# Kernel optimization log

Measured on AMD Instinct MI355X. Metric: run time of the kernel, lower is better.

Reference implementation:

```python
import jax, jax.numpy as jnp
import numpy as np

KS, STRIDE, DIL = 5, 1, 1
PAD = (KS + (KS - 1) * (DIL - 1) - 1) // 2
EPS = 1e-5


def _unfold_t(x):
    # x: (N, C, T, V) -> (N, C, T_out, KS, V), zero-padded temporal windows
    N, C, T, V = x.shape
    xp = jnp.pad(x, ((0, 0), (0, 0), (PAD, PAD), (0, 0)))
    t_out = (T + 2 * PAD - DIL * (KS - 1) - 1) // STRIDE + 1
    idx = jnp.arange(t_out)[:, None] * STRIDE + jnp.arange(KS)[None, :] * DIL  # (T_out, KS)
    return xp[:, :, idx, :]


def _bn2d(x, g, b):
    # training-mode BatchNorm2d: biased batch stats over (N, T, V)
    mu = jnp.mean(x, axis=(0, 2, 3), keepdims=True)
    var = jnp.var(x, axis=(0, 2, 3), keepdims=True)
    xn = (x - mu) * jax.lax.rsqrt(var + EPS)
    return xn * g[None, :, None, None] + b[None, :, None, None]


def setup_inputs() -> dict:
    key = jax.random.key(0)
    ks = jax.random.split(key, 8)
    N, C, T, V = 64, 64, 128, 25
    R, O = 8, 128
    s = 0.05
    return {
        "x": jax.random.normal(ks[0], (N, C, T, V), jnp.float32),
        "Wv": jax.random.normal(ks[1], (R, C), jnp.float32) * s,
        "bv": jax.random.normal(ks[2], (R,), jnp.float32) * s,
        "Ww": jax.random.normal(ks[3], (KS * KS, KS), jnp.float32) * s,
        "bw": jax.random.normal(ks[4], (KS * KS,), jnp.float32) * s,
        "g_bn": jnp.ones((R,), jnp.float32),
        "b_bn": jnp.zeros((R,), jnp.float32),
        "Wr": jax.random.normal(ks[5], (R, C), jnp.float32) * s,
        "br": jax.random.normal(ks[6], (R,), jnp.float32) * s,
        "g_r": jnp.ones((R,), jnp.float32),
        "b_r": jnp.zeros((R,), jnp.float32),
        "Wo": jax.random.normal(ks[7], (O, R), jnp.float32) * s,
        "bo": jnp.zeros((O,), jnp.float32),
        "g_o": jnp.ones((O,), jnp.float32),
        "b_o": jnp.zeros((O,), jnp.float32),
    }


def reference(x, Wv, bv, Ww, bw, g_bn, b_bn, Wr, br, g_r, b_r, Wo, bo, g_o, b_o):
    N, C, T, V = x.shape
    # convV (1x1) then unfold both x and v
    v0 = jnp.einsum('rc,nctv->nrtv', Wv, x) + bv[None, :, None, None]
    xu = _unfold_t(x)      # (N, C, T, W, V)
    vu = _unfold_t(v0)     # (N, R, T, W, V)
    # mean over channels, move window dim to channel position for convW
    m = jnp.mean(xu, axis=1).transpose(0, 2, 1, 3)  # (N, W, T, V)
    w = jnp.einsum('ow,nwtv->notv', Ww, m) + bw[None, :, None, None]
    weights = jnp.tanh(w.reshape(N, KS, KS, T, V))  # (N, W, W, T, V)
    att = jnp.einsum('nwutv,nctuv->nctv', weights, vu)  # (N, R, T, V)
    # residual 1x1 conv + BN (in_channels != out_channels -> conv path)
    res = _bn2d(jnp.einsum('rc,nctv->nrtv', Wr, x) + br[None, :, None, None], g_r, b_r)
    h = _bn2d(att, g_bn, b_bn) + res
    h = jnp.where(h >= 0, h, 0.1 * h)  # LeakyReLU(0.1)
    out = _bn2d(jnp.einsum('or,nrtv->notv', Wo, h) + bo[None, :, None, None], g_o, b_o)
    return out
```

## Files before the change

### kernel.cpp

```cpp
#include <hip/hip_runtime.h>
#include <math.h>

#define TV 3200
#define NTV 204800
#define NB 800
constexpr float EPSF = 1e-5f;

template<int NS>
__device__ inline void write_partials(float (&vals)[NS], float* __restrict__ out, float* lds){
  int lane = threadIdx.x & 63;
  int wid  = threadIdx.x >> 6;
  #pragma unroll
  for (int s = 0; s < NS; ++s){
    float v = vals[s];
    #pragma unroll
    for (int o = 32; o > 0; o >>= 1) v += __shfl_down(v, o);
    if (lane == 0) lds[s*4 + wid] = v;
  }
  __syncthreads();
  if ((int)threadIdx.x < NS){
    float v = lds[threadIdx.x*4+0] + lds[threadIdx.x*4+1]
            + lds[threadIdx.x*4+2] + lds[threadIdx.x*4+3];
    out[threadIdx.x*NB + blockIdx.x] = v;
  }
}

__global__ __launch_bounds__(256) void k_proj(const float* __restrict__ x,
    const float* __restrict__ Wv, const float* __restrict__ bv,
    const float* __restrict__ Wr, const float* __restrict__ br,
    float* __restrict__ v0, float* __restrict__ r0, float* __restrict__ s,
    float* __restrict__ pr){
  __shared__ float sWv[512], sWr[512], lds[16*4];
  int tid = threadIdx.x;
  for (int i = tid; i < 512; i += 256){ sWv[i] = Wv[i]; sWr[i] = Wr[i]; }
  __syncthreads();
  int p = blockIdx.x*256 + tid;
  int n = p / TV, tv = p - n*TV;
  const float* xp = x + (size_t)n*64*TV + tv;
  float av[8] = {0,0,0,0,0,0,0,0};
  float ar[8] = {0,0,0,0,0,0,0,0};
  float ssum = 0.f;
  for (int c = 0; c < 64; ++c){
    float xv = xp[(size_t)c*TV];
    ssum += xv;
    #pragma unroll
    for (int r = 0; r < 8; ++r){
      av[r] = fmaf(sWv[r*64+c], xv, av[r]);
      ar[r] = fmaf(sWr[r*64+c], xv, ar[r]);
    }
  }
  s[p] = ssum * 0.015625f;
  float* v0p = v0 + (size_t)n*8*TV + tv;
  float* r0p = r0 + (size_t)n*8*TV + tv;
  float vals[16];
  #pragma unroll
  for (int r = 0; r < 8; ++r){
    v0p[(size_t)r*TV] = av[r] + bv[r];
    float rr = ar[r] + br[r];
    r0p[(size_t)r*TV] = rr;
    vals[r] = rr; vals[8+r] = rr*rr;
  }
  write_partials<16>(vals, pr, lds);
}

__global__ __launch_bounds__(256) void k_w2(const float* __restrict__ s,
    const float* __restrict__ Ww, const float* __restrict__ bw,
    float* __restrict__ W2){
  __shared__ float sWw[125], sbw[25];
  int tid = threadIdx.x;
  if (tid < 125) sWw[tid] = Ww[tid];
  if (tid < 25)  sbw[tid] = bw[tid];
  __syncthreads();
  int p = blockIdx.x*256 + tid;
  int n = p / TV, tv = p - n*TV;
  int t = tv / 25, v = tv - t*25;
  float m[5];
  #pragma unroll
  for (int k = 0; k < 5; ++k){
    int tt = t + k - 2;
    m[k] = (tt >= 0 && tt < 128) ? s[n*TV + tt*25 + v] : 0.f;
  }
  float w2[5] = {0,0,0,0,0};
  #pragma unroll
  for (int w = 0; w < 5; ++w){
    #pragma unroll
    for (int u = 0; u < 5; ++u){
      int o = w*5 + u;
      float wo = sbw[o];
      #pragma unroll
      for (int k = 0; k < 5; ++k) wo = fmaf(sWw[o*5+k], m[k], wo);
      w2[u] += tanhf(wo);
    }
  }
  float* W2p = W2 + (size_t)n*5*TV + tv;
  #pragma unroll
  for (int u = 0; u < 5; ++u) W2p[(size_t)u*TV] = w2[u];
}

__global__ __launch_bounds__(256) void k_att(const float* __restrict__ W2,
    const float* __restrict__ v0, float* __restrict__ att, float* __restrict__ patt){
  __shared__ float lds[16*4];
  int tid = threadIdx.x;
  int p = blockIdx.x*256 + tid;
  int n = p / TV, tv = p - n*TV;
  int t = tv / 25, v = tv - t*25;
  float a[8] = {0,0,0,0,0,0,0,0};
  const float* W2p = W2 + (size_t)n*5*TV + tv;
  const float* v0n = v0 + (size_t)n*8*TV;
  #pragma unroll
  for (int u = 0; u < 5; ++u){
    int tt = t + u - 2;
    if (tt >= 0 && tt < 128){
      float wu = W2p[(size_t)u*TV];
      const float* vp = v0n + tt*25 + v;
      #pragma unroll
      for (int r = 0; r < 8; ++r) a[r] = fmaf(wu, vp[(size_t)r*TV], a[r]);
    }
  }
  float* ap = att + (size_t)n*8*TV + tv;
  float vals[16];
  #pragma unroll
  for (int r = 0; r < 8; ++r){
    ap[(size_t)r*TV] = a[r];
    vals[r] = a[r]; vals[8+r] = a[r]*a[r];
  }
  write_partials<16>(vals, patt, lds);
}

__global__ __launch_bounds__(256) void k_bncoef(const float* __restrict__ pr,
    const float* __restrict__ patt,
    const float* __restrict__ g_bn, const float* __restrict__ b_bn,
    const float* __restrict__ g_r, const float* __restrict__ b_r,
    float* __restrict__ coef){
  __shared__ float lds[8];
  int b = blockIdx.x;
  bool isatt = (b >= 8);
  int r = isatt ? b - 8 : b;
  const float* ps = (isatt ? patt : pr) + r*NB;
  const float* pq = (isatt ? patt : pr) + (8+r)*NB;
  float s1 = 0.f, s2 = 0.f;
  for (int i = threadIdx.x; i < NB; i += 256){ s1 += ps[i]; s2 += pq[i]; }
  int lane = threadIdx.x & 63, wid = threadIdx.x >> 6;
  #pragma unroll
  for (int o = 32; o > 0; o >>= 1){ s1 += __shfl_down(s1, o); s2 += __shfl_down(s2, o); }
  if (lane == 0){ lds[wid] = s1; lds[4+wid] = s2; }
  __syncthreads();
  if (threadIdx.x == 0){
    float sum = lds[0]+lds[1]+lds[2]+lds[3];
    float sq  = lds[4]+lds[5]+lds[6]+lds[7];
    float mu  = sum / (float)NTV;
    float var = sq / (float)NTV - mu*mu;
    float g  = isatt ? g_bn[r] : g_r[r];
    float bb = isatt ? b_bn[r] : b_r[r];
    float a = g * rsqrtf(var + EPSF);
    float c = bb - a*mu;
    int base = isatt ? 0 : 16;
    coef[base + r] = a;
    coef[base + 8 + r] = c;
  }
}

__global__ __launch_bounds__(256) void k_h(const float* __restrict__ att,
    const float* __restrict__ r0, const float* __restrict__ coef,
    float* __restrict__ h, float* __restrict__ ph){
  __shared__ float lds[44*4];
  __shared__ float sc[32];
  int tid = threadIdx.x;
  if (tid < 32) sc[tid] = coef[tid];
  __syncthreads();
  int p = blockIdx.x*256 + tid;
  int n = p / TV, tv = p - n*TV;
  const float* ap = att + (size_t)n*8*TV + tv;
  const float* rp = r0  + (size_t)n*8*TV + tv;
  float* hp = h + (size_t)n*8*TV + tv;
  float hv[8];
  #pragma unroll
  for (int r = 0; r < 8; ++r){
    float z = sc[r]*ap[(size_t)r*TV] + sc[8+r] + sc[16+r]*rp[(size_t)r*TV] + sc[24+r];
    hv[r] = (z >= 0.f) ? z : 0.1f*z;
    hp[(size_t)r*TV] = hv[r];
  }
  float vals[44];
  #pragma unroll
  for (int r = 0; r < 8; ++r) vals[r] = hv[r];
  int cnt = 8;
  #pragma unroll
  for (int r = 0; r < 8; ++r){
    #pragma unroll
    for (int r2 = r; r2 < 8; ++r2) vals[cnt++] = hv[r]*hv[r2];
  }
  write_partials<44>(vals, ph, lds);
}

__global__ __launch_bounds__(256) void k_hred(const float* __restrict__ ph,
    float* __restrict__ hstat){
  __shared__ float lds[4];
  int j = blockIdx.x;
  float s1 = 0.f;
  for (int i = threadIdx.x; i < NB; i += 256) s1 += ph[j*NB + i];
  int lane = threadIdx.x & 63, wid = threadIdx.x >> 6;
  #pragma unroll
  for (int o = 32; o > 0; o >>= 1) s1 += __shfl_down(s1, o);
  if (lane == 0) lds[wid] = s1;
  __syncthreads();
  if (threadIdx.x == 0) hstat[j] = lds[0]+lds[1]+lds[2]+lds[3];
}

__global__ __launch_bounds__(128) void k_fold(const float* __restrict__ hstat,
    const float* __restrict__ Wo, const float* __restrict__ bo,
    const float* __restrict__ g_o, const float* __restrict__ b_o,
    float* __restrict__ fold, float* __restrict__ bfold){
  __shared__ double muh[8];
  __shared__ double exx[8][8];
  int o = threadIdx.x;
  if (o < 8) muh[o] = (double)hstat[o] / (double)NTV;
  if (o == 0){
    int cnt = 8;
    for (int r = 0; r < 8; ++r)
      for (int r2 = r; r2 < 8; ++r2){
        double e = (double)hstat[cnt++] / (double)NTV;
        exx[r][r2] = e; exx[r2][r] = e;
      }
  }
  __syncthreads();
  double w[8];
  for (int r = 0; r < 8; ++r) w[r] = (double)Wo[o*8+r];
  double bob = (double)bo[o];
  double mu = bob;
  for (int r = 0; r < 8; ++r) mu += w[r]*muh[r];
  double t = 0.0;
  for (int r = 0; r < 8; ++r)
    for (int r2 = 0; r2 < 8; ++r2) t += w[r]*w[r2]*exx[r][r2];
  double ey2 = t + 2.0*bob*(mu - bob) + bob*bob;
  double var = ey2 - mu*mu;
  double a = (double)g_o[o] / sqrt(var + (double)EPSF);
  for (int r = 0; r < 8; ++r) fold[o*8+r] = (float)(a * w[r]);
  bfold[o] = (float)(a * (bob - mu) + (double)b_o[o]);
}

__global__ __launch_bounds__(256) void k_out(const float* __restrict__ h,
    const float* __restrict__ fold, const float* __restrict__ bfold,
    float* __restrict__ out){
  __shared__ float sW[1024], sB[128];
  int tid = threadIdx.x;
  for (int i = tid; i < 1024; i += 256) sW[i] = fold[i];
  if (tid < 128) sB[tid] = bfold[tid];
  __syncthreads();
  int p = blockIdx.x*256 + tid;
  int n = p / TV, tv = p - n*TV;
  const float* hp = h + (size_t)n*8*TV + tv;
  float hv[8];
  #pragma unroll
  for (int r = 0; r < 8; ++r) hv[r] = hp[(size_t)r*TV];
  float* op = out + (size_t)n*128*TV + tv;
  #pragma unroll 4
  for (int o = 0; o < 128; ++o){
    float y = sB[o];
    #pragma unroll
    for (int r = 0; r < 8; ++r) y = fmaf(sW[o*8+r], hv[r], y);
    op[(size_t)o*TV] = y;
  }
}

extern "C" void kernel_launch(void* const* d_in, const int* in_sizes, int n_in,
                              void* d_out, int out_size, void* d_ws, size_t ws_size,
                              hipStream_t stream){
  const float* x    = (const float*)d_in[0];
  const float* Wv   = (const float*)d_in[1];
  const float* bv   = (const float*)d_in[2];
  const float* Ww   = (const float*)d_in[3];
  const float* bw   = (const float*)d_in[4];
  const float* g_bn = (const float*)d_in[5];
  const float* b_bn = (const float*)d_in[6];
  const float* Wr   = (const float*)d_in[7];
  const float* br   = (const float*)d_in[8];
  const float* g_r  = (const float*)d_in[9];
  const float* b_r  = (const float*)d_in[10];
  const float* Wo   = (const float*)d_in[11];
  const float* bo   = (const float*)d_in[12];
  const float* g_o  = (const float*)d_in[13];
  const float* b_o  = (const float*)d_in[14];

  float* ws = (float*)d_ws;
  size_t off = 0;
  float* v0   = ws + off; off += 1638400;
  float* r0   = ws + off; off += 1638400;
  float* s    = ws + off; off += 204800;
  float* W2   = ws + off; off += 1024000;
  float* att  = ws + off; off += 1638400;
  float* hbuf = ws + off; off += 1638400;
  float* pr   = ws + off; off += 16*NB;
  float* patt = ws + off; off += 16*NB;
  float* ph   = ws + off; off += 44*NB;
  float* coef = ws + off; off += 32;
  float* hstat= ws + off; off += 44;
  float* fold = ws + off; off += 1024;
  float* bfold= ws + off; off += 128;

  k_proj  <<<NB, 256, 0, stream>>>(x, Wv, bv, Wr, br, v0, r0, s, pr);
  k_w2    <<<NB, 256, 0, stream>>>(s, Ww, bw, W2);
  k_att   <<<NB, 256, 0, stream>>>(W2, v0, att, patt);
  k_bncoef<<<16, 256, 0, stream>>>(pr, patt, g_bn, b_bn, g_r, b_r, coef);
  k_h     <<<NB, 256, 0, stream>>>(att, r0, coef, hbuf, ph);
  k_hred  <<<44, 256, 0, stream>>>(ph, hstat);
  k_fold  <<<1, 128, 0, stream>>>(hstat, Wo, bo, g_o, b_o, fold, bfold);
  k_out   <<<NB, 256, 0, stream>>>(hbuf, fold, bfold, (float*)d_out);
}
```

Baseline: 240.7 us.

## Fuse attention-weight and attention kernels, vectorize with float4, merge reductions

Fuses the tanh weight computation into the attention kernel using an LDS tile of s and v0 with halo, removing the W2 intermediate buffer. Vectorizes the projection, h and output kernels to process four positions per thread with float4 loads and stores, and splits the output kernel across a second grid dimension over output channels. Merges the h-statistics reduction into the fold kernel, removing a launch. This cuts global traffic and launch count, at the cost of fewer blocks, more registers per thread and redundant halo loads.

```diff
diff --git a/kernel.cpp b/kernel.cpp
--- a/kernel.cpp
+++ b/kernel.cpp
@@ -3,128 +3,154 @@
 
 #define TV 3200
 #define NTV 204800
-#define NB 800
+#define NB 400
 constexpr float EPSF = 1e-5f;
 
 template<int NS>
-__device__ inline void write_partials(float (&vals)[NS], float* __restrict__ out, float* lds){
-  int lane = threadIdx.x & 63;
-  int wid  = threadIdx.x >> 6;
-  #pragma unroll
-  for (int s = 0; s < NS; ++s){
-    float v = vals[s];
+__device__ inline void partials2(const float (&vals)[NS], float* lds, float* out, int ncols){
+  int lane = threadIdx.x & 63, wid = threadIdx.x >> 6;
+  #pragma unroll
+  for (int j = 0; j < NS; ++j){
+    float v = vals[j];
     #pragma unroll
     for (int o = 32; o > 0; o >>= 1) v += __shfl_down(v, o);
-    if (lane == 0) lds[s*4 + wid] = v;
-  }
-  __syncthreads();
-  if ((int)threadIdx.x < NS){
-    float v = lds[threadIdx.x*4+0] + lds[threadIdx.x*4+1]
-            + lds[threadIdx.x*4+2] + lds[threadIdx.x*4+3];
-    out[threadIdx.x*NB + blockIdx.x] = v;
-  }
-}
-
-__global__ __launch_bounds__(256) void k_proj(const float* __restrict__ x,
-    const float* __restrict__ Wv, const float* __restrict__ bv,
+    if (lane == 0) lds[j*2 + wid] = v;
+  }
+  __syncthreads();
+  if ((int)threadIdx.x < NS)
+    out[threadIdx.x*ncols + blockIdx.x] = lds[threadIdx.x*2] + lds[threadIdx.x*2 + 1];
+}
+
+__global__ __launch_bounds__(128, 2) void k_proj(
+    const float* __restrict__ x, const float* __restrict__ Wv, const float* __restrict__ bv,
     const float* __restrict__ Wr, const float* __restrict__ br,
     float* __restrict__ v0, float* __restrict__ r0, float* __restrict__ s,
     float* __restrict__ pr){
-  __shared__ float sWv[512], sWr[512], lds[16*4];
-  int tid = threadIdx.x;
-  for (int i = tid; i < 512; i += 256){ sWv[i] = Wv[i]; sWr[i] = Wr[i]; }
-  __syncthreads();
-  int p = blockIdx.x*256 + tid;
-  int n = p / TV, tv = p - n*TV;
-  const float* xp = x + (size_t)n*64*TV + tv;
-  float av[8] = {0,0,0,0,0,0,0,0};
-  float ar[8] = {0,0,0,0,0,0,0,0};
-  float ssum = 0.f;
+  __shared__ __align__(16) float sW[1024];
+  __shared__ float lds[32];
+  const int tid = threadIdx.x;
+  for (int i = tid; i < 1024; i += 128){
+    int c = i >> 4, j = i & 15;
+    sW[i] = (j < 8) ? Wv[j*64 + c] : Wr[(j-8)*64 + c];
+  }
+  __syncthreads();
+  const int p4 = (blockIdx.x*128 + tid) * 4;
+  const int n = p4 / TV, tv4 = p4 - n*TV;
+  const float* xb = x + (size_t)n*64*TV + tv4;
+  float4 av[8], ar[8];
+  #pragma unroll
+  for (int r = 0; r < 8; ++r){
+    av[r] = make_float4(0.f,0.f,0.f,0.f);
+    ar[r] = make_float4(0.f,0.f,0.f,0.f);
+  }
+  float4 ss = make_float4(0.f,0.f,0.f,0.f);
+  #pragma unroll 8
   for (int c = 0; c < 64; ++c){
-    float xv = xp[(size_t)c*TV];
-    ssum += xv;
+    float4 xv = *(const float4*)(xb + (size_t)c*TV);
+    ss.x += xv.x; ss.y += xv.y; ss.z += xv.z; ss.w += xv.w;
     #pragma unroll
     for (int r = 0; r < 8; ++r){
-      av[r] = fmaf(sWv[r*64+c], xv, av[r]);
-      ar[r] = fmaf(sWr[r*64+c], xv, ar[r]);
-    }
-  }
-  s[p] = ssum * 0.015625f;
-  float* v0p = v0 + (size_t)n*8*TV + tv;
-  float* r0p = r0 + (size_t)n*8*TV + tv;
+      float wv = sW[c*16 + r], wr = sW[c*16 + 8 + r];
+      av[r].x = fmaf(wv, xv.x, av[r].x); av[r].y = fmaf(wv, xv.y, av[r].y);
+      av[r].z = fmaf(wv, xv.z, av[r].z); av[r].w = fmaf(wv, xv.w, av[r].w);
+      ar[r].x = fmaf(wr, xv.x, ar[r].x); ar[r].y = fmaf(wr, xv.y, ar[r].y);
+      ar[r].z = fmaf(wr, xv.z, ar[r].z); ar[r].w = fmaf(wr, xv.w, ar[r].w);
+    }
+  }
+  *(float4*)(s + p4) = make_float4(ss.x*0.015625f, ss.y*0.015625f, ss.z*0.015625f, ss.w*0.015625f);
   float vals[16];
   #pragma unroll
   for (int r = 0; r < 8; ++r){
-    v0p[(size_t)r*TV] = av[r] + bv[r];
-    float rr = ar[r] + br[r];
-    r0p[(size_t)r*TV] = rr;
-    vals[r] = rr; vals[8+r] = rr*rr;
-  }
-  write_partials<16>(vals, pr, lds);
-}
-
-__global__ __launch_bounds__(256) void k_w2(const float* __restrict__ s,
-    const float* __restrict__ Ww, const float* __restrict__ bw,
-    float* __restrict__ W2){
-  __shared__ float sWw[125], sbw[25];
-  int tid = threadIdx.x;
+    float bvr = bv[r], brr = br[r];
+    float4 vv = make_float4(av[r].x+bvr, av[r].y+bvr, av[r].z+bvr, av[r].w+bvr);
+    *(float4*)(v0 + (size_t)r*NTV + p4) = vv;
+    float4 rr = make_float4(ar[r].x+brr, ar[r].y+brr, ar[r].z+brr, ar[r].w+brr);
+    *(float4*)(r0 + (size_t)r*NTV + p4) = rr;
+    vals[r]   = rr.x + rr.y + rr.z + rr.w;
+    vals[8+r] = rr.x*rr.x + rr.y*rr.y + rr.z*rr.z + rr.w*rr.w;
+  }
+  partials2<16>(vals, lds, pr, NB);
+}
+
+__global__ __launch_bounds__(128, 2) void k_att(
+    const float* __restrict__ s, const float* __restrict__ Ww, const float* __restrict__ bw,
+    const float* __restrict__ v0, float* __restrict__ att, float* __restrict__ patt){
+  __shared__ __align__(16) float sS[616];
+  __shared__ __align__(16) float sV[8*616];
+  __shared__ float sWw[128], sbw[32];
+  __shared__ float lds[32];
+  const int tid = threadIdx.x;
   if (tid < 125) sWw[tid] = Ww[tid];
   if (tid < 25)  sbw[tid] = bw[tid];
-  __syncthreads();
-  int p = blockIdx.x*256 + tid;
-  int n = p / TV, tv = p - n*TV;
-  int t = tv / 25, v = tv - t*25;
-  float m[5];
-  #pragma unroll
-  for (int k = 0; k < 5; ++k){
-    int tt = t + k - 2;
-    m[k] = (tt >= 0 && tt < 128) ? s[n*TV + tt*25 + v] : 0.f;
-  }
-  float w2[5] = {0,0,0,0,0};
-  #pragma unroll
-  for (int w = 0; w < 5; ++w){
+  const int P0 = blockIdx.x * 512;
+  const int base = P0 - 52;
+  for (int i = tid; i < 154; i += 128){
+    int q = base + i*4;
+    float4 val;
+    if (q >= 0 && q + 3 < NTV) val = *(const float4*)(s + q);
+    else {
+      float tmp[4];
+      #pragma unroll
+      for (int j = 0; j < 4; ++j){ int qe = q + j; tmp[j] = (qe >= 0 && qe < NTV) ? s[qe] : 0.f; }
+      val = make_float4(tmp[0], tmp[1], tmp[2], tmp[3]);
+    }
+    *(float4*)&sS[i*4] = val;
+  }
+  for (int i = tid; i < 1232; i += 128){
+    int r = i / 154, j = i - r*154;
+    int q = base + j*4;
+    const float* vr = v0 + (size_t)r*NTV;
+    float4 val;
+    if (q >= 0 && q + 3 < NTV) val = *(const float4*)(vr + q);
+    else {
+      float tmp[4];
+      #pragma unroll
+      for (int jj = 0; jj < 4; ++jj){ int qe = q + jj; tmp[jj] = (qe >= 0 && qe < NTV) ? vr[qe] : 0.f; }
+      val = make_float4(tmp[0], tmp[1], tmp[2], tmp[3]);
+    }
+    *(float4*)&sV[r*616 + j*4] = val;
+  }
+  __syncthreads();
+  float vals[16];
+  #pragma unroll
+  for (int j = 0; j < 16; ++j) vals[j] = 0.f;
+  #pragma unroll
+  for (int e = 0; e < 4; ++e){
+    const int p = P0 + e*128 + tid;
+    const int n = p / TV, tv = p - n*TV;
+    const int li0 = e*128 + tid + 52;
+    float m[5];
+    #pragma unroll
+    for (int k = 0; k < 5; ++k){
+      int q = tv + (k-2)*25;
+      m[k] = (q >= 0 && q < TV) ? sS[li0 + (k-2)*25] : 0.f;
+    }
+    float acc[8] = {0.f,0.f,0.f,0.f,0.f,0.f,0.f,0.f};
     #pragma unroll
     for (int u = 0; u < 5; ++u){
-      int o = w*5 + u;
-      float wo = sbw[o];
+      float w2u = 0.f;
       #pragma unroll
-      for (int k = 0; k < 5; ++k) wo = fmaf(sWw[o*5+k], m[k], wo);
-      w2[u] += tanhf(wo);
-    }
-  }
-  float* W2p = W2 + (size_t)n*5*TV + tv;
-  #pragma unroll
-  for (int u = 0; u < 5; ++u) W2p[(size_t)u*TV] = w2[u];
-}
-
-__global__ __launch_bounds__(256) void k_att(const float* __restrict__ W2,
-    const float* __restrict__ v0, float* __restrict__ att, float* __restrict__ patt){
-  __shared__ float lds[16*4];
-  int tid = threadIdx.x;
-  int p = blockIdx.x*256 + tid;
-  int n = p / TV, tv = p - n*TV;
-  int t = tv / 25, v = tv - t*25;
-  float a[8] = {0,0,0,0,0,0,0,0};
-  const float* W2p = W2 + (size_t)n*5*TV + tv;
-  const float* v0n = v0 + (size_t)n*8*TV;
-  #pragma unroll
-  for (int u = 0; u < 5; ++u){
-    int tt = t + u - 2;
-    if (tt >= 0 && tt < 128){
-      float wu = W2p[(size_t)u*TV];
-      const float* vp = v0n + tt*25 + v;
-      #pragma unroll
-      for (int r = 0; r < 8; ++r) a[r] = fmaf(wu, vp[(size_t)r*TV], a[r]);
-    }
-  }
-  float* ap = att + (size_t)n*8*TV + tv;
-  float vals[16];
-  #pragma unroll
-  for (int r = 0; r < 8; ++r){
-    ap[(size_t)r*TV] = a[r];
-    vals[r] = a[r]; vals[8+r] = a[r]*a[r];
-  }
-  write_partials<16>(vals, patt, lds);
+      for (int w = 0; w < 5; ++w){
+        int o = w*5 + u;
+        float z = sbw[o];
+        #pragma unroll
+        for (int k = 0; k < 5; ++k) z = fmaf(sWw[o*5+k], m[k], z);
+        w2u += tanhf(z);
+      }
+      int q = tv + (u-2)*25;
+      if (q >= 0 && q < TV){
+        int li = li0 + (u-2)*25;
+        #pragma unroll
+        for (int r = 0; r < 8; ++r) acc[r] = fmaf(w2u, sV[r*616 + li], acc[r]);
+      }
+    }
+    #pragma unroll
+    for (int r = 0; r < 8; ++r){
+      att[(size_t)r*NTV + p] = acc[r];
+      vals[r] += acc[r]; vals[8+r] += acc[r]*acc[r];
+    }
+  }
+  partials2<16>(vals, lds, patt, NB);
 }
 
 __global__ __launch_bounds__(256) void k_bncoef(const float* __restrict__ pr,
@@ -135,7 +161,7 @@
   __shared__ float lds[8];
   int b = blockIdx.x;
   bool isatt = (b >= 8);
-  int r = isatt ? b - 8 : b;
+  int r = b & 7;
   const float* ps = (isatt ? patt : pr) + r*NB;
   const float* pq = (isatt ? patt : pr) + (8+r)*NB;
   float s1 = 0.f, s2 = 0.f;
@@ -153,112 +179,126 @@
     float g  = isatt ? g_bn[r] : g_r[r];
     float bb = isatt ? b_bn[r] : b_r[r];
     float a = g * rsqrtf(var + EPSF);
-    float c = bb - a*mu;
-    int base = isatt ? 0 : 16;
-    coef[base + r] = a;
-    coef[base + 8 + r] = c;
-  }
-}
-
-__global__ __launch_bounds__(256) void k_h(const float* __restrict__ att,
-    const float* __restrict__ r0, const float* __restrict__ coef,
-    float* __restrict__ h, float* __restrict__ ph){
-  __shared__ float lds[44*4];
+    int b0 = isatt ? 0 : 16;
+    coef[b0 + r] = a;
+    coef[b0 + 8 + r] = bb - a*mu;
+  }
+}
+
+__global__ __launch_bounds__(128, 2) void k_h(
+    const float* __restrict__ att, const float* __restrict__ r0,
+    const float* __restrict__ coef, float* __restrict__ h, float* __restrict__ ph){
   __shared__ float sc[32];
-  int tid = threadIdx.x;
+  __shared__ float lds[96];
+  const int tid = threadIdx.x;
   if (tid < 32) sc[tid] = coef[tid];
   __syncthreads();
-  int p = blockIdx.x*256 + tid;
-  int n = p / TV, tv = p - n*TV;
-  const float* ap = att + (size_t)n*8*TV + tv;
-  const float* rp = r0  + (size_t)n*8*TV + tv;
-  float* hp = h + (size_t)n*8*TV + tv;
-  float hv[8];
+  const int p4 = (blockIdx.x*128 + tid) * 4;
+  float4 hv[8];
+  float vals[44];
   #pragma unroll
   for (int r = 0; r < 8; ++r){
-    float z = sc[r]*ap[(size_t)r*TV] + sc[8+r] + sc[16+r]*rp[(size_t)r*TV] + sc[24+r];
-    hv[r] = (z >= 0.f) ? z : 0.1f*z;
-    hp[(size_t)r*TV] = hv[r];
-  }
-  float vals[44];
-  #pragma unroll
-  for (int r = 0; r < 8; ++r) vals[r] = hv[r];
+    float4 a = *(const float4*)(att + (size_t)r*NTV + p4);
+    float4 b = *(const float4*)(r0  + (size_t)r*NTV + p4);
+    float ca = sc[r], cb = sc[8+r], cc = sc[16+r], cd = sc[24+r];
+    float4 z;
+    z.x = ca*a.x + cb + cc*b.x + cd;
+    z.y = ca*a.y + cb + cc*b.y + cd;
+    z.z = ca*a.z + cb + cc*b.z + cd;
+    z.w = ca*a.w + cb + cc*b.w + cd;
+    hv[r].x = (z.x >= 0.f) ? z.x : 0.1f*z.x;
+    hv[r].y = (z.y >= 0.f) ? z.y : 0.1f*z.y;
+    hv[r].z = (z.z >= 0.f) ? z.z : 0.1f*z.z;
+    hv[r].w = (z.w >= 0.f) ? z.w : 0.1f*z.w;
+    *(float4*)(h + (size_t)r*NTV + p4) = hv[r];
+    vals[r] = hv[r].x + hv[r].y + hv[r].z + hv[r].w;
+  }
   int cnt = 8;
   #pragma unroll
-  for (int r = 0; r < 8; ++r){
-    #pragma unroll
-    for (int r2 = r; r2 < 8; ++r2) vals[cnt++] = hv[r]*hv[r2];
-  }
-  write_partials<44>(vals, ph, lds);
-}
-
-__global__ __launch_bounds__(256) void k_hred(const float* __restrict__ ph,
-    float* __restrict__ hstat){
-  __shared__ float lds[4];
-  int j = blockIdx.x;
-  float s1 = 0.f;
-  for (int i = threadIdx.x; i < NB; i += 256) s1 += ph[j*NB + i];
-  int lane = threadIdx.x & 63, wid = threadIdx.x >> 6;
-  #pragma unroll
-  for (int o = 32; o > 0; o >>= 1) s1 += __shfl_down(s1, o);
-  if (lane == 0) lds[wid] = s1;
-  __syncthreads();
-  if (threadIdx.x == 0) hstat[j] = lds[0]+lds[1]+lds[2]+lds[3];
-}
-
-__global__ __launch_bounds__(128) void k_fold(const float* __restrict__ hstat,
+  for (int r = 0; r < 8; ++r)
+    #pragma unroll
+    for (int r2 = r; r2 < 8; ++r2){
+      vals[cnt++] = hv[r].x*hv[r2].x + hv[r].y*hv[r2].y + hv[r].z*hv[r2].z + hv[r].w*hv[r2].w;
+    }
+  partials2<44>(vals, lds, ph, NB);
+}
+
+__global__ __launch_bounds__(256) void k_foldred(const float* __restrict__ ph,
     const float* __restrict__ Wo, const float* __restrict__ bo,
     const float* __restrict__ g_o, const float* __restrict__ b_o,
     float* __restrict__ fold, float* __restrict__ bfold){
+  __shared__ float sm[176];
+  __shared__ float s44[44];
   __shared__ double muh[8];
-  __shared__ double exx[8][8];
-  int o = threadIdx.x;
-  if (o < 8) muh[o] = (double)hstat[o] / (double)NTV;
-  if (o == 0){
+  __shared__ double exx[64];
+  const int tid = threadIdx.x;
+  if (tid < 176){
+    int j = tid >> 2, q = tid & 3;
+    const float* row = ph + j*NB + q*100;
+    float acc = 0.f;
+    for (int i = 0; i < 100; ++i) acc += row[i];
+    sm[tid] = acc;
+  }
+  __syncthreads();
+  if (tid < 44) s44[tid] = sm[4*tid] + sm[4*tid+1] + sm[4*tid+2] + sm[4*tid+3];
+  __syncthreads();
+  if (tid < 8) muh[tid] = (double)s44[tid] / (double)NTV;
+  if (tid == 0){
     int cnt = 8;
     for (int r = 0; r < 8; ++r)
       for (int r2 = r; r2 < 8; ++r2){
-        double e = (double)hstat[cnt++] / (double)NTV;
-        exx[r][r2] = e; exx[r2][r] = e;
+        double e = (double)s44[cnt++] / (double)NTV;
+        exx[r*8+r2] = e; exx[r2*8+r] = e;
       }
   }
   __syncthreads();
-  double w[8];
-  for (int r = 0; r < 8; ++r) w[r] = (double)Wo[o*8+r];
-  double bob = (double)bo[o];
-  double mu = bob;
-  for (int r = 0; r < 8; ++r) mu += w[r]*muh[r];
-  double t = 0.0;
-  for (int r = 0; r < 8; ++r)
-    for (int r2 = 0; r2 < 8; ++r2) t += w[r]*w[r2]*exx[r][r2];
-  double ey2 = t + 2.0*bob*(mu - bob) + bob*bob;
-  double var = ey2 - mu*mu;
-  double a = (double)g_o[o] / sqrt(var + (double)EPSF);
-  for (int r = 0; r < 8; ++r) fold[o*8+r] = (float)(a * w[r]);
-  bfold[o] = (float)(a * (bob - mu) + (double)b_o[o]);
+  if (tid < 128){
+    double w[8];
+    #pragma unroll
+    for (int r = 0; r < 8; ++r) w[r] = (double)Wo[tid*8+r];
+    double bob = (double)bo[tid];
+    double mu = bob;
+    for (int r = 0; r < 8; ++r) mu += w[r]*muh[r];
+    double t2 = 0.0;
+    for (int r = 0; r < 8; ++r)
+      for (int r2 = 0; r2 < 8; ++r2) t2 += w[r]*w[r2]*exx[r*8+r2];
+    double ey2 = t2 + 2.0*bob*(mu - bob) + bob*bob;
+    double var = ey2 - mu*mu;
+    double a = (double)g_o[tid] / sqrt(var + (double)EPSF);
+    #pragma unroll
+    for (int r = 0; r < 8; ++r) fold[tid*8+r] = (float)(a * w[r]);
+    bfold[tid] = (float)(a * (bob - mu) + (double)b_o[tid]);
+  }
 }
 
 __global__ __launch_bounds__(256) void k_out(const float* __restrict__ h,
     const float* __restrict__ fold, const float* __restrict__ bfold,
     float* __restrict__ out){
-  __shared__ float sW[1024], sB[128];
-  int tid = threadIdx.x;
-  for (int i = tid; i < 1024; i += 256) sW[i] = fold[i];
-  if (tid < 128) sB[tid] = bfold[tid];
-  __syncthreads();
-  int p = blockIdx.x*256 + tid;
-  int n = p / TV, tv = p - n*TV;
-  const float* hp = h + (size_t)n*8*TV + tv;
-  float hv[8];
-  #pragma unroll
-  for (int r = 0; r < 8; ++r) hv[r] = hp[(size_t)r*TV];
-  float* op = out + (size_t)n*128*TV + tv;
+  __shared__ float sW[256], sB[32];
+  const int tid = threadIdx.x;
+  const int yo = blockIdx.y * 32;
+  sW[tid] = fold[yo*8 + tid];
+  if (tid < 32) sB[tid] = bfold[yo + tid];
+  __syncthreads();
+  const int p4 = (blockIdx.x*256 + tid) * 4;
+  const int n = p4 / TV, tv4 = p4 - n*TV;
+  float4 hv[8];
+  #pragma unroll
+  for (int r = 0; r < 8; ++r) hv[r] = *(const float4*)(h + (size_t)r*NTV + p4);
+  float* ob = out + (size_t)n*128*TV + tv4;
   #pragma unroll 4
-  for (int o = 0; o < 128; ++o){
-    float y = sB[o];
-    #pragma unroll
-    for (int r = 0; r < 8; ++r) y = fmaf(sW[o*8+r], hv[r], y);
-    op[(size_t)o*TV] = y;
+  for (int o = 0; o < 32; ++o){
+    float b = sB[o];
+    float4 y = make_float4(b, b, b, b);
+    #pragma unroll
+    for (int r = 0; r < 8; ++r){
+      float w = sW[o*8+r];
+      y.x = fmaf(w, hv[r].x, y.x);
+      y.y = fmaf(w, hv[r].y, y.y);
+      y.z = fmaf(w, hv[r].z, y.z);
+      y.w = fmaf(w, hv[r].w, y.w);
+    }
+    *(float4*)(ob + (size_t)(yo + o)*TV) = y;
   }
 }
 
@@ -283,26 +323,22 @@
 
   float* ws = (float*)d_ws;
   size_t off = 0;
-  float* v0   = ws + off; off += 1638400;
-  float* r0   = ws + off; off += 1638400;
-  float* s    = ws + off; off += 204800;
-  float* W2   = ws + off; off += 1024000;
-  float* att  = ws + off; off += 1638400;
-  float* hbuf = ws + off; off += 1638400;
+  float* v0   = ws + off; off += 8*NTV;
+  float* r0   = ws + off; off += 8*NTV;
+  float* s    = ws + off; off += NTV;
+  float* att  = ws + off; off += 8*NTV;
+  float* hbuf = ws + off; off += 8*NTV;
   float* pr   = ws + off; off += 16*NB;
   float* patt = ws + off; off += 16*NB;
   float* ph   = ws + off; off += 44*NB;
   float* coef = ws + off; off += 32;
-  float* hstat= ws + off; off += 44;
   float* fold = ws + off; off += 1024;
   float* bfold= ws + off; off += 128;
 
-  k_proj  <<<NB, 256, 0, stream>>>(x, Wv, bv, Wr, br, v0, r0, s, pr);
-  k_w2    <<<NB, 256, 0, stream>>>(s, Ww, bw, W2);
-  k_att   <<<NB, 256, 0, stream>>>(W2, v0, att, patt);
-  k_bncoef<<<16, 256, 0, stream>>>(pr, patt, g_bn, b_bn, g_r, b_r, coef);
-  k_h     <<<NB, 256, 0, stream>>>(att, r0, coef, hbuf, ph);
-  k_hred  <<<44, 256, 0, stream>>>(ph, hstat);
-  k_fold  <<<1, 128, 0, stream>>>(hstat, Wo, bo, g_o, b_o, fold, bfold);
-  k_out   <<<NB, 256, 0, stream>>>(hbuf, fold, bfold, (float*)d_out);
-}
+  k_proj   <<<NB, 128, 0, stream>>>(x, Wv, bv, Wr, br, v0, r0, s, pr);
+  k_att    <<<NB, 128, 0, stream>>>(s, Ww, bw, v0, att, patt);
+  k_bncoef <<<16, 256, 0, stream>>>(pr, patt, g_bn, b_bn, g_r, b_r, coef);
+  k_h      <<<NB, 128, 0, stream>>>(att, r0, coef, hbuf, ph);
+  k_foldred<<<1, 256, 0, stream>>>(ph, Wo, bo, g_o, b_o, fold, bfold);
+  k_out    <<<dim3(200, 4), 256, 0, stream>>>(hbuf, fold, bfold, (float*)d_out);
+}
```

Result: slower. 262.8 us (+9.2%).
